# Optimization experiments

Hardware: AMD Instinct MI355X
Metric: run time of the kernel (lower is better)

## Reference

```python
import jax, jax.numpy as jnp
import numpy as np

NUM_HEADS = 32


def setup_inputs() -> dict:
    key = jax.random.key(0)
    ks = jax.random.split(key, 6)
    B, S, D = 1, 2048, 4096
    hd = D // NUM_HEADS  # 128
    x = jax.random.normal(ks[0], (B, S, D), dtype=jnp.float32)
    # true rotary frequencies: freqs_cis = exp(i * t * theta^{-2j/hd})
    inv_freq = 1.0 / (10000.0 ** (jnp.arange(0, hd, 2, dtype=jnp.float32) / hd))  # [hd//2]
    angles = jnp.arange(S, dtype=jnp.float32)[:, None] * inv_freq[None, :]  # [S, hd//2]
    freqs_cos = jnp.cos(angles)
    freqs_sin = jnp.sin(angles)
    scale = 0.02
    wq = jax.random.normal(ks[1], (D, D), dtype=jnp.float32) * scale
    wk = jax.random.normal(ks[2], (D, D), dtype=jnp.float32) * scale
    wv = jax.random.normal(ks[3], (D, D), dtype=jnp.float32) * scale
    wo = jax.random.normal(ks[4], (D, D), dtype=jnp.float32) * scale
    return {"x": x, "freqs_cos": freqs_cos, "freqs_sin": freqs_sin,
            "wq": wq, "wk": wk, "wv": wv, "wo": wo}


def _apply_rope(t, cos, sin):
    # t: [B, S, H, hd]; cos/sin: [S, hd//2]
    B, S, H, hd = t.shape
    tr = t.reshape(B, S, H, hd // 2, 2)
    a, b = tr[..., 0], tr[..., 1]
    c = cos[None, :, None, :]
    s = sin[None, :, None, :]
    out_r = a * c - b * s
    out_i = a * s + b * c
    return jnp.stack([out_r, out_i], axis=-1).reshape(B, S, H, hd)


def reference(x, freqs_cos, freqs_sin, wq, wk, wv, wo):
    B, S, D = x.shape
    H = NUM_HEADS
    hd = D // H
    xq = (x @ wq).reshape(B, S, H, hd)
    xk = (x @ wk).reshape(B, S, H, hd)
    xv = (x @ wv).reshape(B, S, H, hd)
    xq = _apply_rope(xq, freqs_cos, freqs_sin)
    xk = _apply_rope(xk, freqs_cos, freqs_sin)
    # [B, H, S, hd]
    xq = xq.transpose(0, 2, 1, 3)
    xk = xk.transpose(0, 2, 1, 3)
    xv = xv.transpose(0, 2, 1, 3)
    scores = jnp.einsum('bhqd,bhkd->bhqk', xq, xk) / jnp.sqrt(jnp.float32(hd))
    scores = jax.nn.softmax(scores.astype(jnp.float32), axis=-1).astype(xq.dtype)
    out = jnp.einsum('bhqk,bhkd->bhqd', scores, xv)
    out = out.transpose(0, 2, 1, 3).reshape(B, S, D)
    return out @ wo
```

## Files before the change

kernel.cpp:

```cpp
#include <hip/hip_runtime.h>
#include <hip/hip_bf16.h>

typedef __hip_bfloat16 bf16;
typedef __attribute__((ext_vector_type(8))) short short8;
typedef __attribute__((ext_vector_type(4))) short short4v;
typedef __attribute__((ext_vector_type(4))) float f32x4;

#define MFMA16(a, b, c) __builtin_amdgcn_mfma_f32_16x16x32_bf16((a), (b), (c), 0, 0, 0)

static __device__ __forceinline__ void gload_lds16(const bf16* g, bf16* l) {
  __builtin_amdgcn_global_load_lds((const __attribute__((address_space(1))) unsigned int*)g,
                                   (__attribute__((address_space(3))) unsigned int*)l,
                                   16, 0, 0);
}

__global__ __launch_bounds__(256) void castx_kernel(const float* __restrict__ x,
                                                    bf16* __restrict__ xb, int n) {
  int i = (blockIdx.x * 256 + threadIdx.x) * 8;
  if (i >= n) return;
  float4 v0 = *(const float4*)(x + i);
  float4 v1 = *(const float4*)(x + i + 4);
  bf16 tmp[8];
  tmp[0] = __float2bfloat16(v0.x); tmp[1] = __float2bfloat16(v0.y);
  tmp[2] = __float2bfloat16(v0.z); tmp[3] = __float2bfloat16(v0.w);
  tmp[4] = __float2bfloat16(v1.x); tmp[5] = __float2bfloat16(v1.y);
  tmp[6] = __float2bfloat16(v1.z); tmp[7] = __float2bfloat16(v1.w);
  *(short8*)(xb + i) = *(short8*)tmp;
}

__global__ __launch_bounds__(256) void tw_kernel(const float* __restrict__ W,
                                                 bf16* __restrict__ WT) {
  __shared__ bf16 tile[64][65];
  int b = blockIdx.x;
  int tk = (b >> 6) * 64;
  int tn = (b & 63) * 64;
  int t = threadIdx.x;
  int c = t & 63, r0 = t >> 6;
#pragma unroll
  for (int i = 0; i < 16; ++i) {
    int r = i * 4 + r0;
    tile[c][r] = __float2bfloat16(W[(size_t)(tk + r) * 4096 + tn + c]);
  }
  __syncthreads();
#pragma unroll
  for (int i = 0; i < 16; ++i) {
    int r = i * 4 + r0;
    WT[(size_t)(tn + r) * 4096 + tk + c] = tile[r][c];
  }
}

template <int EPI>
__global__ __launch_bounds__(512) void gemm8(const bf16* __restrict__ A,
                                             const bf16* __restrict__ Bt,
                                             void* __restrict__ Cv,
                                             void* __restrict__ Cv2,
                                             int M, int N,
                                             const float* __restrict__ fcos,
                                             const float* __restrict__ fsin) {
  __shared__ bf16 LDS[2 * 32768];
  const int K = 4096, NK = 64;
  const int NB = N >> 8;
  int g = blockIdx.x;
  int nwg = (M >> 8) * NB;
  int wid = (g & 7) * (nwg >> 3) + (g >> 3);
  int bm = wid / NB, bn = wid % NB;
  int t = threadIdx.x, lane = t & 63, w = t >> 6;
  int wm = w >> 2, wn = w & 3;
  int lr = lane & 15, lg = lane >> 4;
  int rsw = (lr >> 1) & 3;
  f32x4 acc[8][4] = {};

  const bf16* Ab = A + (size_t)bm * 256 * K;
  const bf16* Bb = Bt + (size_t)bn * 256 * K;
  int sr4 = t >> 2;
  int sg = (t & 3) ^ ((t >> 3) & 3);

#define SA(nb, kt2, kh)                                                          \
  do {                                                                           \
    _Pragma("unroll") for (int j = 0; j < 2; ++j)                                \
      gload_lds16(Ab + (size_t)(j * 128 + sr4) * K + (kt2) * 64 + (kh) * 32 + sg * 8, \
                  LDS + (nb) + (kh) * 8192 + (j * 512 + t) * 8);                 \
  } while (0)
#define SB(nb, kt2, kh)                                                          \
  do {                                                                           \
    _Pragma("unroll") for (int j = 0; j < 2; ++j)                                \
      gload_lds16(Bb + (size_t)(j * 128 + sr4) * K + (kt2) * 64 + (kh) * 32 + sg * 8, \
                  LDS + (nb) + 16384 + (kh) * 8192 + (j * 512 + t) * 8);         \
  } while (0)
#define AFR(base, kc, mi) \
  (*(const short8*)(LDS + (base) + (kc) * 8192 + (wm * 128 + (mi) * 16 + lr) * 32 + ((lg ^ rsw) << 3)))
#define BFR(base, kc, nf) \
  (*(const short8*)(LDS + (base) + 16384 + (kc) * 8192 + (wn * 64 + (nf) * 16 + lr) * 32 + ((lg ^ rsw) << 3)))

  SA(0, 0, 0); SB(0, 0, 0); SA(0, 0, 1); SB(0, 0, 1);
  asm volatile("s_waitcnt vmcnt(4)" ::: "memory");
  __builtin_amdgcn_s_barrier();

  int cur = 0;
  for (int kt = 0; kt < NK; ++kt) {
    int base = cur * 32768;
    int nbf = (cur ^ 1) * 32768;
    bool pf = (kt + 1) < NK;
    short8 a[4], b[4];

#pragma unroll
    for (int nf = 0; nf < 4; ++nf) b[nf] = BFR(base, 0, nf);
#pragma unroll
    for (int i = 0; i < 4; ++i) a[i] = AFR(base, 0, i);
    if (pf) SA(nbf, kt + 1, 0);
    __builtin_amdgcn_s_barrier();
    __builtin_amdgcn_s_setprio(1);
#pragma unroll
    for (int i = 0; i < 4; ++i)
#pragma unroll
      for (int nf = 0; nf < 4; ++nf)
        acc[i][nf] = MFMA16(a[i], b[nf], acc[i][nf]);
    __builtin_amdgcn_s_setprio(0);
    __builtin_amdgcn_s_barrier();

#pragma unroll
    for (int i = 0; i < 4; ++i) a[i] = AFR(base, 0, 4 + i);
    if (pf) SB(nbf, kt + 1, 0);
    __builtin_amdgcn_s_barrier();
    __builtin_amdgcn_s_setprio(1);
#pragma unroll
    for (int i = 0; i < 4; ++i)
#pragma unroll
      for (int nf = 0; nf < 4; ++nf)
        acc[4 + i][nf] = MFMA16(a[i], b[nf], acc[4 + i][nf]);
    __builtin_amdgcn_s_setprio(0);
    if (pf)
      asm volatile("s_waitcnt vmcnt(4)" ::: "memory");
    else
      asm volatile("s_waitcnt vmcnt(0)" ::: "memory");
    __builtin_amdgcn_s_barrier();

#pragma unroll
    for (int nf = 0; nf < 4; ++nf) b[nf] = BFR(base, 1, nf);
#pragma unroll
    for (int i = 0; i < 4; ++i) a[i] = AFR(base, 1, i);
    if (pf) SA(nbf, kt + 1, 1);
    __builtin_amdgcn_s_barrier();
    __builtin_amdgcn_s_setprio(1);
#pragma unroll
    for (int i = 0; i < 4; ++i)
#pragma unroll
      for (int nf = 0; nf < 4; ++nf)
        acc[i][nf] = MFMA16(a[i], b[nf], acc[i][nf]);
    __builtin_amdgcn_s_setprio(0);
    __builtin_amdgcn_s_barrier();

#pragma unroll
    for (int i = 0; i < 4; ++i) a[i] = AFR(base, 1, 4 + i);
    if (pf) SB(nbf, kt + 1, 1);
    __builtin_amdgcn_s_barrier();
    __builtin_amdgcn_s_setprio(1);
#pragma unroll
    for (int i = 0; i < 4; ++i)
#pragma unroll
      for (int nf = 0; nf < 4; ++nf)
        acc[4 + i][nf] = MFMA16(a[i], b[nf], acc[4 + i][nf]);
    __builtin_amdgcn_s_setprio(0);
    asm volatile("s_waitcnt vmcnt(4)" ::: "memory");
    __builtin_amdgcn_s_barrier();

    cur ^= 1;
  }
#undef SA
#undef SB
#undef AFR
#undef BFR

#pragma unroll
  for (int mi = 0; mi < 8; ++mi)
#pragma unroll
    for (int nf = 0; nf < 4; ++nf) {
      int row0 = bm * 256 + wm * 128 + mi * 16 + lg * 4;
      if constexpr (EPI == 1) {
        int sect = bn >> 4, bnl = bn & 15;
        bf16* Cb = sect ? (bf16*)Cv2 : (bf16*)Cv;
        const float qs = sect ? 1.0f : 0.08838834764831845f;
        int col = bnl * 256 + wn * 64 + nf * 16 + lr;
        int ip = (col >> 1) & 63;
        float sgn = (col & 1) ? 1.0f : -1.0f;
#pragma unroll
        for (int r = 0; r < 4; ++r) {
          int row = row0 + r;
          float mine = acc[mi][nf][r];
          float oth = __shfl_xor(mine, 1);
          float cv = fcos[row * 64 + ip];
          float sv = fsin[row * 64 + ip];
          float v = (mine * cv + sgn * oth * sv) * qs;
          Cb[(size_t)row * 4096 + col] = __float2bfloat16(v);
        }
      } else if constexpr (EPI == 3) {
        int col = bn * 256 + wn * 64 + nf * 16 + lr;
        bf16 tmp[4];
#pragma unroll
        for (int r = 0; r < 4; ++r) tmp[r] = __float2bfloat16(acc[mi][nf][r]);
        *(short4v*)((bf16*)Cv + (size_t)col * M + row0) = *(short4v*)tmp;
      } else {
        int col = bn * 256 + wn * 64 + nf * 16 + lr;
#pragma unroll
        for (int r = 0; r < 4; ++r) {
          int row = row0 + r;
          ((float*)Cv)[(size_t)row * N + col] = acc[mi][nf][r];
        }
      }
    }
}

__global__ __launch_bounds__(512, 2) void attn_fwd(const bf16* __restrict__ Q,
                                                   const bf16* __restrict__ K,
                                                   const bf16* __restrict__ Vt,
                                                   bf16* __restrict__ O) {
  __shared__ bf16 Kbuf[2][64 * 128];
  __shared__ bf16 Vbuf[2][128 * 64];
  __shared__ char Ps_all[8][2][2048];
  const int S = 2048, D = 4096, HD = 128, NT = 32;
  int g = blockIdx.y * 8 + blockIdx.x;
  int wid = (g & 7) * 32 + (g >> 3);
  int h = wid >> 3, qb = wid & 7;
  int tid = threadIdx.x, lane = tid & 63, w = tid >> 6;
  int lr = lane & 15, lg = lane >> 4;
  int q0 = qb * 256 + w * 32;
  int swz = (lr & 7) << 4;

  const bf16* Kh = K + h * HD;
  const bf16* Vh = Vt + (size_t)h * HD * S;

  short8 aq[2][4];
#pragma unroll
  for (int u = 0; u < 2; ++u)
#pragma unroll
    for (int c = 0; c < 4; ++c)
      aq[u][c] = *(const short8*)(Q + (size_t)(q0 + u * 16 + lr) * D + h * HD + c * 32 + lg * 8);

  int kr = lane >> 4, ksl = lane & 15;
  int vr = lane >> 3, vsl = lane & 7;

  f32x4 accO[2][8] = {};
  float lsum[2] = {0.f, 0.f};

#define STAGE(b, ttile)                                                            \
  do {                                                                             \
    int kv0_ = (ttile) * 64;                                                       \
    _Pragma("unroll") for (int ii = 0; ii < 2; ++ii) {                             \
      int row = w * 8 + ii * 4 + kr;                                               \
      gload_lds16(Kh + (size_t)(kv0_ + row) * D + ((ksl ^ (row & 7)) << 3),        \
                  &Kbuf[b][(w * 8 + ii * 4) * 128]);                               \
    }                                                                              \
    _Pragma("unroll") for (int ii = 0; ii < 2; ++ii) {                             \
      int row = w * 16 + ii * 8 + vr;                                              \
      gload_lds16(Vh + (size_t)row * S + kv0_ + ((vsl ^ (row & 7)) << 3),          \
                  &Vbuf[b][(w * 16 + ii * 8) * 64]);                               \
    }                                                                              \
  } while (0)

  int cur = 0;
  STAGE(0, 0);
  for (int tt = 0; tt < NT; ++tt) {
    if (tt + 1 < NT) {
      STAGE(cur ^ 1, tt + 1);
      asm volatile("s_waitcnt vmcnt(4)" ::: "memory");
    } else {
      asm volatile("s_waitcnt vmcnt(0)" ::: "memory");
    }
    __builtin_amdgcn_s_barrier();
    const bf16* Kb_ = Kbuf[cur];
    const bf16* Vb_ = Vbuf[cur];

    f32x4 sf[2][4] = {};
#pragma unroll
    for (int j = 0; j < 4; ++j)
#pragma unroll
      for (int c = 0; c < 4; ++c) {
        short8 kf = *(const short8*)(Kb_ + (j * 16 + lr) * 128 +
                                     (((c * 4 + lg) ^ (lr & 7)) << 3));
        sf[0][j] = MFMA16(kf, aq[0][c], sf[0][j]);
        sf[1][j] = MFMA16(kf, aq[1][c], sf[1][j]);
      }
#pragma unroll
    for (int u = 0; u < 2; ++u) {
      char* Ps = Ps_all[w][u];
#pragma unroll
      for (int j = 0; j < 4; ++j) {
        float p0 = __expf(sf[u][j][0]);
        float p1 = __expf(sf[u][j][1]);
        float p2 = __expf(sf[u][j][2]);
        float p3 = __expf(sf[u][j][3]);
        lsum[u] += (p0 + p1) + (p2 + p3);
        bf16 pk[4] = {__float2bfloat16(p0), __float2bfloat16(p1),
                      __float2bfloat16(p2), __float2bfloat16(p3)};
        *(short4v*)(Ps + lr * 128 + ((j * 32 + lg * 8) ^ swz)) = *(short4v*)pk;
      }
    }
#pragma unroll
    for (int t2 = 0; t2 < 2; ++t2) {
      short8 pa0 = *(const short8*)(Ps_all[w][0] + lr * 128 + ((t2 * 64 + lg * 16) ^ swz));
      short8 pa1 = *(const short8*)(Ps_all[w][1] + lr * 128 + ((t2 * 64 + lg * 16) ^ swz));
#pragma unroll
      for (int n = 0; n < 8; ++n) {
        short8 bv = *(const short8*)(Vb_ + (n * 16 + lr) * 64 +
                                     (((t2 * 4 + lg) ^ (lr & 7)) << 3));
        accO[0][n] = MFMA16(pa0, bv, accO[0][n]);
        accO[1][n] = MFMA16(pa1, bv, accO[1][n]);
      }
    }
    __builtin_amdgcn_s_barrier();
    cur ^= 1;
  }
#undef STAGE

#pragma unroll
  for (int u = 0; u < 2; ++u) {
    float ls = lsum[u];
    ls += __shfl_xor(ls, 16);
    ls += __shfl_xor(ls, 32);
    float rs[4];
#pragma unroll
    for (int r = 0; r < 4; ++r)
      rs[r] = 1.f / __shfl(ls, lg * 4 + r);
#pragma unroll
    for (int n = 0; n < 8; ++n)
#pragma unroll
      for (int r = 0; r < 4; ++r) {
        int row = q0 + u * 16 + lg * 4 + r;
        int col = h * HD + n * 16 + lr;
        O[(size_t)row * D + col] = __float2bfloat16(accO[u][n][r] * rs[r]);
      }
  }
}

extern "C" void kernel_launch(void* const* d_in, const int* in_sizes, int n_in,
                              void* d_out, int out_size, void* d_ws, size_t ws_size,
                              hipStream_t stream) {
  const float* x    = (const float*)d_in[0];
  const float* fcos = (const float*)d_in[1];
  const float* fsin = (const float*)d_in[2];
  const float* wq   = (const float*)d_in[3];
  const float* wk   = (const float*)d_in[4];
  const float* wv   = (const float*)d_in[5];
  const float* wo   = (const float*)d_in[6];
  float* out = (float*)d_out;

  const int S = 2048, D = 4096;
  const size_t MB = 1024 * 1024;
  char* ws = (char*)d_ws;
  bf16* xb  = (bf16*)(ws);
  bf16* wT2 = (bf16*)(ws + 16 * MB);
  bf16* Vt  = (bf16*)(ws + 48 * MB);
  bf16* Qb  = (bf16*)(ws + 80 * MB);
  bf16* Kb  = (bf16*)(ws + 96 * MB);
  bf16* AO  = (bf16*)(ws);

  int n = S * D;
  castx_kernel<<<n / (256 * 8), 256, 0, stream>>>(x, xb, n);

  tw_kernel<<<4096, 256, 0, stream>>>(wq, wT2);
  tw_kernel<<<4096, 256, 0, stream>>>(wk, wT2 + (size_t)4096 * 4096);
  gemm8<1><<<256, 512, 0, stream>>>(xb, wT2, Qb, Kb, S, 8192, fcos, fsin);

  tw_kernel<<<4096, 256, 0, stream>>>(wv, wT2);
  gemm8<3><<<128, 512, 0, stream>>>(xb, wT2, Vt, nullptr, S, D, nullptr, nullptr);

  attn_fwd<<<dim3(8, 32), 512, 0, stream>>>(Qb, Kb, Vt, AO);

  tw_kernel<<<4096, 256, 0, stream>>>(wo, wT2);
  gemm8<4><<<128, 512, 0, stream>>>(AO, wT2, out, nullptr, S, D, nullptr, nullptr);
}
```

Measured before the change: 482.4 us.

## Use 128x256 tiles for V/O GEMMs, drop intra-iteration barriers, remap XCD tiles

```diff
diff --git a/kernel.cpp b/kernel.cpp
--- a/kernel.cpp
+++ b/kernel.cpp
@@ -49,21 +49,18 @@
   }
 }
 
-template <int EPI>
-__global__ __launch_bounds__(512) void gemm8(const bf16* __restrict__ A,
-                                             const bf16* __restrict__ Bt,
-                                             void* __restrict__ Cv,
-                                             void* __restrict__ Cv2,
-                                             int M, int N,
-                                             const float* __restrict__ fcos,
-                                             const float* __restrict__ fsin) {
+__global__ __launch_bounds__(512) void gemmQK8(const bf16* __restrict__ A,
+                                               const bf16* __restrict__ Bt,
+                                               bf16* __restrict__ Qb,
+                                               bf16* __restrict__ Kb,
+                                               const float* __restrict__ fcos,
+                                               const float* __restrict__ fsin) {
   __shared__ bf16 LDS[2 * 32768];
   const int K = 4096, NK = 64;
-  const int NB = N >> 8;
   int g = blockIdx.x;
-  int nwg = (M >> 8) * NB;
-  int wid = (g & 7) * (nwg >> 3) + (g >> 3);
-  int bm = wid / NB, bn = wid % NB;
+  int xcd = g & 7, loc = g >> 3;
+  int bm = (xcd >> 2) * 4 + (loc >> 3);
+  int bn = (xcd & 3) * 8 + (loc & 7);
   int t = threadIdx.x, lane = t & 63, w = t >> 6;
   int wm = w >> 2, wn = w & 3;
   int lr = lane & 15, lg = lane >> 4;
@@ -108,7 +105,6 @@
 #pragma unroll
     for (int i = 0; i < 4; ++i) a[i] = AFR(base, 0, i);
     if (pf) SA(nbf, kt + 1, 0);
-    __builtin_amdgcn_s_barrier();
     __builtin_amdgcn_s_setprio(1);
 #pragma unroll
     for (int i = 0; i < 4; ++i)
@@ -116,12 +112,9 @@
       for (int nf = 0; nf < 4; ++nf)
         acc[i][nf] = MFMA16(a[i], b[nf], acc[i][nf]);
     __builtin_amdgcn_s_setprio(0);
-    __builtin_amdgcn_s_barrier();
-
 #pragma unroll
     for (int i = 0; i < 4; ++i) a[i] = AFR(base, 0, 4 + i);
     if (pf) SB(nbf, kt + 1, 0);
-    __builtin_amdgcn_s_barrier();
     __builtin_amdgcn_s_setprio(1);
 #pragma unroll
     for (int i = 0; i < 4; ++i)
@@ -140,7 +133,6 @@
 #pragma unroll
     for (int i = 0; i < 4; ++i) a[i] = AFR(base, 1, i);
     if (pf) SA(nbf, kt + 1, 1);
-    __builtin_amdgcn_s_barrier();
     __builtin_amdgcn_s_setprio(1);
 #pragma unroll
     for (int i = 0; i < 4; ++i)
@@ -148,12 +140,9 @@
       for (int nf = 0; nf < 4; ++nf)
         acc[i][nf] = MFMA16(a[i], b[nf], acc[i][nf]);
     __builtin_amdgcn_s_setprio(0);
-    __builtin_amdgcn_s_barrier();
-
 #pragma unroll
     for (int i = 0; i < 4; ++i) a[i] = AFR(base, 1, 4 + i);
     if (pf) SB(nbf, kt + 1, 1);
-    __builtin_amdgcn_s_barrier();
     __builtin_amdgcn_s_setprio(1);
 #pragma unroll
     for (int i = 0; i < 4; ++i)
@@ -171,41 +160,129 @@
 #undef AFR
 #undef BFR
 
+  int sect = bn >> 4, bnl = bn & 15;
+  bf16* Cb = sect ? Kb : Qb;
+  const float qs = sect ? 1.0f : 0.08838834764831845f;
 #pragma unroll
   for (int mi = 0; mi < 8; ++mi)
 #pragma unroll
     for (int nf = 0; nf < 4; ++nf) {
+      int col = bnl * 256 + wn * 64 + nf * 16 + lr;
       int row0 = bm * 256 + wm * 128 + mi * 16 + lg * 4;
-      if constexpr (EPI == 1) {
-        int sect = bn >> 4, bnl = bn & 15;
-        bf16* Cb = sect ? (bf16*)Cv2 : (bf16*)Cv;
-        const float qs = sect ? 1.0f : 0.08838834764831845f;
-        int col = bnl * 256 + wn * 64 + nf * 16 + lr;
-        int ip = (col >> 1) & 63;
-        float sgn = (col & 1) ? 1.0f : -1.0f;
-#pragma unroll
-        for (int r = 0; r < 4; ++r) {
-          int row = row0 + r;
-          float mine = acc[mi][nf][r];
-          float oth = __shfl_xor(mine, 1);
-          float cv = fcos[row * 64 + ip];
-          float sv = fsin[row * 64 + ip];
-          float v = (mine * cv + sgn * oth * sv) * qs;
-          Cb[(size_t)row * 4096 + col] = __float2bfloat16(v);
-        }
-      } else if constexpr (EPI == 3) {
-        int col = bn * 256 + wn * 64 + nf * 16 + lr;
+      int ip = (col >> 1) & 63;
+      float sgn = (col & 1) ? 1.0f : -1.0f;
+#pragma unroll
+      for (int r = 0; r < 4; ++r) {
+        int row = row0 + r;
+        float mine = acc[mi][nf][r];
+        float oth = __shfl_xor(mine, 1);
+        float cv = fcos[row * 64 + ip];
+        float sv = fsin[row * 64 + ip];
+        float v = (mine * cv + sgn * oth * sv) * qs;
+        Cb[(size_t)row * 4096 + col] = __float2bfloat16(v);
+      }
+    }
+}
+
+template <int EPI>
+__global__ __launch_bounds__(512) void gemmB(const bf16* __restrict__ A,
+                                             const bf16* __restrict__ Bt,
+                                             void* __restrict__ Cv,
+                                             int M, int N) {
+  __shared__ bf16 LDS[2 * 24576];
+  const int K = 4096, NK = 64;
+  int g = blockIdx.x;
+  int xcd = g & 7, loc = g >> 3;
+  int bm = (xcd >> 1) * 4 + (loc >> 3);
+  int bn = (xcd & 1) * 8 + (loc & 7);
+  int t = threadIdx.x, lane = t & 63, w = t >> 6;
+  int lr = lane & 15, lg = lane >> 4;
+  int rsw = (lr >> 1) & 3;
+  f32x4 acc[8][2] = {};
+
+  const bf16* Ab = A + (size_t)bm * 128 * K;
+  const bf16* Bb = Bt + (size_t)bn * 256 * K;
+  int sr4 = t >> 2;
+  int sg = (t & 3) ^ ((t >> 3) & 3);
+
+#define SAB(nb, kt2, kh)                                                         \
+  gload_lds16(Ab + (size_t)sr4 * K + (kt2) * 64 + (kh) * 32 + sg * 8,            \
+              LDS + (nb) + (kh) * 4096 + t * 8)
+#define SBB(nb, kt2, kh)                                                         \
+  do {                                                                           \
+    _Pragma("unroll") for (int j = 0; j < 2; ++j)                                \
+      gload_lds16(Bb + (size_t)(j * 128 + sr4) * K + (kt2) * 64 + (kh) * 32 + sg * 8, \
+                  LDS + (nb) + 8192 + (kh) * 8192 + (j * 512 + t) * 8);          \
+  } while (0)
+#define AFRB(base, kc, mi) \
+  (*(const short8*)(LDS + (base) + (kc) * 4096 + ((mi) * 16 + lr) * 32 + ((lg ^ rsw) << 3)))
+#define BFRB(base, kc, nf) \
+  (*(const short8*)(LDS + (base) + 8192 + (kc) * 8192 + (w * 32 + (nf) * 16 + lr) * 32 + ((lg ^ rsw) << 3)))
+
+  SAB(0, 0, 0); SBB(0, 0, 0); SAB(0, 0, 1); SBB(0, 0, 1);
+  asm volatile("s_waitcnt vmcnt(3)" ::: "memory");
+  __builtin_amdgcn_s_barrier();
+
+  int cur = 0;
+  for (int kt = 0; kt < NK; ++kt) {
+    int base = cur * 24576;
+    int nbf = (cur ^ 1) * 24576;
+    bool pf = (kt + 1) < NK;
+    short8 a[8], b[2];
+
+    b[0] = BFRB(base, 0, 0); b[1] = BFRB(base, 0, 1);
+#pragma unroll
+    for (int i = 0; i < 8; ++i) a[i] = AFRB(base, 0, i);
+    if (pf) { SAB(nbf, kt + 1, 0); SBB(nbf, kt + 1, 0); }
+    if (pf)
+      asm volatile("s_waitcnt vmcnt(3)" ::: "memory");
+    else
+      asm volatile("s_waitcnt vmcnt(0)" ::: "memory");
+    __builtin_amdgcn_s_barrier();
+    __builtin_amdgcn_s_setprio(1);
+#pragma unroll
+    for (int i = 0; i < 8; ++i)
+#pragma unroll
+      for (int nf = 0; nf < 2; ++nf)
+        acc[i][nf] = MFMA16(a[i], b[nf], acc[i][nf]);
+    __builtin_amdgcn_s_setprio(0);
+
+    b[0] = BFRB(base, 1, 0); b[1] = BFRB(base, 1, 1);
+#pragma unroll
+    for (int i = 0; i < 8; ++i) a[i] = AFRB(base, 1, i);
+    if (pf) { SAB(nbf, kt + 1, 1); SBB(nbf, kt + 1, 1); }
+    asm volatile("s_waitcnt vmcnt(3)" ::: "memory");
+    __builtin_amdgcn_s_barrier();
+    __builtin_amdgcn_s_setprio(1);
+#pragma unroll
+    for (int i = 0; i < 8; ++i)
+#pragma unroll
+      for (int nf = 0; nf < 2; ++nf)
+        acc[i][nf] = MFMA16(a[i], b[nf], acc[i][nf]);
+    __builtin_amdgcn_s_setprio(0);
+
+    cur ^= 1;
+  }
+#undef SAB
+#undef SBB
+#undef AFRB
+#undef BFRB
+
+#pragma unroll
+  for (int mi = 0; mi < 8; ++mi)
+#pragma unroll
+    for (int nf = 0; nf < 2; ++nf) {
+      int col = bn * 256 + w * 32 + nf * 16 + lr;
+      int row0 = bm * 128 + mi * 16 + lg * 4;
+      if constexpr (EPI == 3) {
         bf16 tmp[4];
 #pragma unroll
         for (int r = 0; r < 4; ++r) tmp[r] = __float2bfloat16(acc[mi][nf][r]);
         *(short4v*)((bf16*)Cv + (size_t)col * M + row0) = *(short4v*)tmp;
       } else {
-        int col = bn * 256 + wn * 64 + nf * 16 + lr;
-#pragma unroll
-        for (int r = 0; r < 4; ++r) {
-          int row = row0 + r;
-          ((float*)Cv)[(size_t)row * N + col] = acc[mi][nf][r];
-        }
+#pragma unroll
+        for (int r = 0; r < 4; ++r)
+          ((float*)Cv)[(size_t)(row0 + r) * N + col] = acc[mi][nf][r];
       }
     }
 }
@@ -359,13 +436,13 @@
 
   tw_kernel<<<4096, 256, 0, stream>>>(wq, wT2);
   tw_kernel<<<4096, 256, 0, stream>>>(wk, wT2 + (size_t)4096 * 4096);
-  gemm8<1><<<256, 512, 0, stream>>>(xb, wT2, Qb, Kb, S, 8192, fcos, fsin);
+  gemmQK8<<<256, 512, 0, stream>>>(xb, wT2, Qb, Kb, fcos, fsin);
 
   tw_kernel<<<4096, 256, 0, stream>>>(wv, wT2);
-  gemm8<3><<<128, 512, 0, stream>>>(xb, wT2, Vt, nullptr, S, D, nullptr, nullptr);
+  gemmB<3><<<256, 512, 0, stream>>>(xb, wT2, Vt, S, D);
 
   attn_fwd<<<dim3(8, 32), 512, 0, stream>>>(Qb, Kb, Vt, AO);
 
   tw_kernel<<<4096, 256, 0, stream>>>(wo, wT2);
-  gemm8<4><<<128, 512, 0, stream>>>(AO, wT2, out, nullptr, S, D, nullptr, nullptr);
-}
+  gemmB<4><<<256, 512, 0, stream>>>(AO, wT2, out, S, D);
+}
```

Result: faster. 410.0 us (-15.0%).
